# Kernel tuning notes

Hardware: AMD Instinct MI355X
Metric: run time of the kernel (lower is better)

The kernel has to match this reference:

```python
import jax, jax.numpy as jnp
import numpy as np

DIM = 192
N_HEADS = 8
HEAD_DIM = DIM // N_HEADS
SCALE = 1.0 / np.sqrt(HEAD_DIM).astype(np.float32)
H_GRID, W_GRID = 32, 64
KH, KW = 7, 11


def build_local_mask():
    # Equivalent to the torch double-loop construction: token (h2,w2) may attend
    # to (h,w) iff |h2-h| <= KH//2 and |w2-w| <= KW//2 (odd kernels).
    hh = jnp.arange(H_GRID)
    ww = jnp.arange(W_GRID)
    dh_ok = jnp.abs(hh[:, None] - hh[None, :]) <= KH // 2  # [H, H]
    dw_ok = jnp.abs(ww[:, None] - ww[None, :]) <= KW // 2  # [W, W]
    allowed = dh_ok[:, None, :, None] & dw_ok[None, :, None, :]  # [H, W, H, W]
    allowed = allowed.reshape(H_GRID * W_GRID, H_GRID * W_GRID)
    return jnp.where(allowed, 0.0, -jnp.inf).astype(jnp.float32)  # [N, N]


def setup_inputs() -> dict:
    key = jax.random.key(0)
    ks = jax.random.split(key, 5)
    B, N = 4, H_GRID * W_GRID
    w_std = 1.0 / np.sqrt(DIM)
    x = jax.random.normal(ks[0], (B, N, DIM), dtype=jnp.float32)
    qkv_w = jax.random.normal(ks[1], (3 * DIM, DIM), dtype=jnp.float32) * w_std
    qkv_b = jax.random.normal(ks[2], (3 * DIM,), dtype=jnp.float32) * 0.02
    proj_w = jax.random.normal(ks[3], (DIM, DIM), dtype=jnp.float32) * w_std
    proj_b = jax.random.normal(ks[4], (DIM,), dtype=jnp.float32) * 0.02
    mask = build_local_mask()
    return {"x": x, "qkv_w": qkv_w, "qkv_b": qkv_b,
            "proj_w": proj_w, "proj_b": proj_b, "mask": mask}


def reference(x, qkv_w, qkv_b, proj_w, proj_b, mask):
    B, N, _ = x.shape
    qkv = x @ qkv_w.T + qkv_b                              # [B, N, 3*DIM]
    qkv = qkv.reshape(B, N, 3, N_HEADS, HEAD_DIM)
    qkv = jnp.transpose(qkv, (2, 0, 3, 1, 4))              # [3, B, h, N, d]
    q, k, v = qkv[0] * SCALE, qkv[1], qkv[2]
    attn = jnp.einsum('bhnd,bhmd->bhnm', q, k) + mask      # [B, h, N, N]
    attn = jax.nn.softmax(attn, axis=-1)                   # == log_softmax().exp()
    out = jnp.einsum('bhnm,bhmd->bhnd', attn, v)           # [B, h, N, d]
    out = jnp.transpose(out, (0, 2, 1, 3)).reshape(B, N, DIM)
    return out @ proj_w.T + proj_b
```

## Files before the change

kernel.cpp:

```cpp
#include <hip/hip_runtime.h>
#include <math.h>

#define H_GRID 32
#define W_GRID 64
#define NTOK   2048
#define NHEADS 8
#define HD     24
#define DIMC   192
#define BATCH  4

static constexpr float SCALE = 0.20412414523193154f;

typedef unsigned short ushort;
typedef unsigned int   uint;
typedef __attribute__((ext_vector_type(8))) _Float16 f16x8;
typedef __attribute__((ext_vector_type(4))) float    f32x4;

static __device__ __forceinline__ float4 ld4(const float* p) { return *(const float4*)p; }

static __device__ __forceinline__ ushort f2h(float f) {
    _Float16 h = (_Float16)f;
    union { _Float16 h; ushort u; } c; c.h = h; return c.u;
}
static __device__ __forceinline__ float h2f(ushort u) {
    union { ushort u; _Float16 h; } c; c.u = u; return (float)c.h;
}

__global__ __launch_bounds__(256) void cast_h(const float* __restrict__ x,
                                              const float* __restrict__ wq,
                                              const float* __restrict__ wp,
                                              ushort* __restrict__ xh,
                                              ushort* __restrict__ wqh,
                                              ushort* __restrict__ wph,
                                              ushort* __restrict__ Qh,
                                              ushort* __restrict__ Kh) {
    const int i = blockIdx.x * 256 + threadIdx.x;
    if (i >= 430080) {
        const int ti = i - 430080;
        ushort* dst = (ti >> 16) ? Kh : Qh;
        const int row = ti & 65535;
        const uint4 z = {0u, 0u, 0u, 0u};
        *(uint4*)&dst[(size_t)row * 32 + 24] = z;
        return;
    }
    const float* src; ushort* dh; int off;
    if (i < 393216)      { src = x;  dh = xh;  off = i; }
    else if (i < 420864) { src = wq; dh = wqh; off = i - 393216; }
    else                 { src = wp; dh = wph; off = i - 420864; }
    float4 v = ld4(src + (size_t)off * 4);
    *(ushort4*)(dh + (size_t)off * 4) =
        make_ushort4(f2h(v.x), f2h(v.y), f2h(v.z), f2h(v.w));
}

__global__ __launch_bounds__(256) void gemm_qkv(const ushort* __restrict__ Ah,
                                                const ushort* __restrict__ Wh,
                                                const float* __restrict__ bias,
                                                ushort* __restrict__ Qh,
                                                ushort* __restrict__ Kh,
                                                ushort* __restrict__ VTh) {
    __shared__ ushort Ws[64 * 200];

    const int t    = threadIdx.x;
    const int wave = t >> 6, lane = t & 63;
    const int m0   = blockIdx.x * 64 + wave * 16;
    const int j0   = blockIdx.y * 64;
    const int n16  = lane & 15;
    const int kq   = lane >> 4;

    for (int i = t; i < 1536; i += 256) {
        const int r = i / 24, c = i - (i / 24) * 24;
        *(uint4*)&Ws[r * 200 + c * 8] = *(const uint4*)&Wh[(size_t)(j0 + r) * 192 + c * 8];
    }

    const ushort* ap = Ah + (size_t)(m0 + n16) * 192 + kq * 8;

    f32x4 acc[4] = {f32x4{0,0,0,0}, f32x4{0,0,0,0}, f32x4{0,0,0,0}, f32x4{0,0,0,0}};

    __syncthreads();

#pragma unroll
    for (int ks = 0; ks < 6; ks++) {
        const f16x8 af = *(const f16x8*)(ap + ks * 32);
#pragma unroll
        for (int nt = 0; nt < 4; nt++) {
            const f16x8 bf = *(const f16x8*)&Ws[(nt * 16 + n16) * 200 + kq * 8 + ks * 32];
            acc[nt] = __builtin_amdgcn_mfma_f32_16x16x32_f16(af, bf, acc[nt], 0, 0, 0);
        }
    }

    const int band = blockIdx.y / 3;
    const int mrow0 = m0 + kq * 4;
    const int b_    = mrow0 >> 11;
    const int tok0  = mrow0 & 2047;

    if (band == 2) {
#pragma unroll
        for (int nt = 0; nt < 4; nt++) {
            const int col = j0 + nt * 16 + n16;
            const int lc  = col - 384;
            const int h_  = lc / 24;
            const int d_  = lc - h_ * 24;
            const float bv = bias[col];
            ushort vv[4];
#pragma unroll
            for (int r = 0; r < 4; r++) vv[r] = f2h(acc[nt][r] + bv);
            const size_t addr = ((size_t)(b_ * 8 + h_) * 32 + d_) * 2080 + 8 + tok0;
            *(ushort4*)&VTh[addr] = make_ushort4(vv[0], vv[1], vv[2], vv[3]);
        }
    } else {
        const float sc_ = band ? 1.0f : SCALE;
        __syncthreads();
#pragma unroll
        for (int nt = 0; nt < 4; nt++) {
            const int col = j0 + nt * 16 + n16;
            const float bv = bias[col];
#pragma unroll
            for (int r = 0; r < 4; r++) {
                Ws[(wave * 16 + kq * 4 + r) * 68 + nt * 16 + n16] =
                    f2h((acc[nt][r] + bv) * sc_);
            }
        }
        __syncthreads();
        ushort* dst = band ? Kh : Qh;
        const int lc0 = j0 - band * 192;
#pragma unroll
        for (int it = 0; it < 4; it++) {
            const int item = t + 256 * it;
            const int tokl = item >> 4;
            const int cg   = item & 15;
            const ushort4 v = *(const ushort4*)&Ws[tokl * 68 + cg * 4];
            const int lc = lc0 + cg * 4;
            const int h_ = lc / 24;
            const int d0 = lc - h_ * 24;
            const int m  = blockIdx.x * 64 + tokl;
            const size_t addr = ((size_t)((m >> 11) * 8 + h_) * 2048 + (m & 2047)) * 32 + d0;
            *(ushort4*)&dst[addr] = v;
        }
    }
}

__global__ __launch_bounds__(256) void attn_mfma(const ushort* __restrict__ Qh,
                                                 const ushort* __restrict__ Kh,
                                                 const ushort* __restrict__ VTh,
                                                 ushort* __restrict__ aws) {
    const int qtile = blockIdx.x;
    const int head  = blockIdx.y;
    const int b     = blockIdx.z;
    const int qh0   = (qtile >> 3) * 4;
    const int qw0   = (qtile & 7) * 8;
    const int kw0a  = qw0 - 8;

    const int t = threadIdx.x;
    const int w = t >> 6, lane = t & 63;
    const int n16 = lane & 15, quad = lane >> 4;
    const int bh = b * 8 + head;

    __shared__ ushort P[32 * 328];
    __shared__ ushort Os[32 * 28];
    __shared__ float  mxbuf[64], sumbuf[64];

    const ushort* Qb = Qh + (size_t)bh * 65536;
    const ushort* Kb = Kh + (size_t)bh * 65536;

    const int mt = w >> 1, nth = w & 1;
    const int mrow = 16 * mt + n16;
    const int tq_a = ((qh0 + (mrow >> 3)) << 6) + qw0 + (mrow & 7);
    const f16x8 qf = *(const f16x8*)&Qb[(size_t)tq_a * 32 + quad * 8];

    float sv[10][4];
    float mx4[4] = {-3e38f, -3e38f, -3e38f, -3e38f};
#pragma unroll
    for (int j = 0; j < 10; j++) {
        const int slot = (nth * 10 + j) * 16 + n16;
        const int rr = slot >> 5, cc = slot & 31;
        const int khv = qh0 - 3 + rr;
        const int kwv = kw0a + cc;
        const int tok = (min(max(khv, 0), 31) << 6) + min(max(kwv, 0), 63);
        const f16x8 kf = *(const f16x8*)&Kb[(size_t)tok * 32 + quad * 8];
        f32x4 a = f32x4{0, 0, 0, 0};
        a = __builtin_amdgcn_mfma_f32_16x16x32_f16(qf, kf, a, 0, 0, 0);
        const bool kok = (khv >= 0) && (khv < 32) && (kwv >= 0) && (kwv < 64);
#pragma unroll
        for (int r = 0; r < 4; r++) {
            const int m   = 16 * mt + quad * 4 + r;
            const int qhv = qh0 + (m >> 3);
            const int qwv = qw0 + (m & 7);
            const bool valid = kok && (abs(khv - qhv) <= 3) && (abs(kwv - qwv) <= 5);
            const float s = valid ? a[r] : -3e38f;
            sv[j][r] = s;
            mx4[r] = fmaxf(mx4[r], s);
        }
    }
#pragma unroll
    for (int d = 1; d < 16; d <<= 1)
#pragma unroll
        for (int r = 0; r < 4; r++) mx4[r] = fmaxf(mx4[r], __shfl_xor(mx4[r], d));
    if (n16 == 0) {
#pragma unroll
        for (int r = 0; r < 4; r++) mxbuf[w * 16 + quad * 4 + r] = mx4[r];
    }
    __syncthreads();
#pragma unroll
    for (int r = 0; r < 4; r++) mx4[r] = fmaxf(mx4[r], mxbuf[(w ^ 1) * 16 + quad * 4 + r]);

    float sum4[4] = {0.f, 0.f, 0.f, 0.f};
#pragma unroll
    for (int j = 0; j < 10; j++) {
        const int slot = (nth * 10 + j) * 16 + n16;
#pragma unroll
        for (int r = 0; r < 4; r++) {
            const float p = __expf(sv[j][r] - mx4[r]);
            const ushort ph = f2h(p);
            sum4[r] += h2f(ph);
            P[(16 * mt + quad * 4 + r) * 328 + slot] = ph;
        }
    }
#pragma unroll
    for (int d = 1; d < 16; d <<= 1)
#pragma unroll
        for (int r = 0; r < 4; r++) sum4[r] += __shfl_xor(sum4[r], d);
    if (n16 == 0) {
#pragma unroll
        for (int r = 0; r < 4; r++) sumbuf[w * 16 + quad * 4 + r] = sum4[r];
    }
    __syncthreads();

    const int mtP = w >> 1, ntP = w & 1;
    const int dcol = 16 * ntP + n16;
    const ushort* VTb = VTh + (size_t)bh * 32 * 2080;
    f32x4 acc = f32x4{0, 0, 0, 0};
#pragma unroll
    for (int ks = 0; ks < 10; ks++) {
        const int kh_cl = min(max(qh0 - 3 + ks, 0), 31);
        const f16x8 pa = *(const f16x8*)&P[(16 * mtP + n16) * 328 + ks * 32 + quad * 8];
        const f16x8 vf = *(const f16x8*)&VTb[(size_t)dcol * 2080 + 8 + (kh_cl << 6) + kw0a + quad * 8];
        acc = __builtin_amdgcn_mfma_f32_16x16x32_f16(pa, vf, acc, 0, 0, 0);
    }
    if (dcol < 24) {
#pragma unroll
        for (int r = 0; r < 4; r++) {
            const int m = 16 * mtP + quad * 4 + r;
            const float tot = sumbuf[(2 * mtP) * 16 + (m & 15)] +
                              sumbuf[(2 * mtP + 1) * 16 + (m & 15)];
            Os[m * 28 + dcol] = f2h(acc[r] / tot);
        }
    }
    __syncthreads();

    if (t < 192) {
        const int tok = t / 6, g = t - (t / 6) * 6;
        const ushort4 v = *(const ushort4*)&Os[tok * 28 + g * 4];
        const int tq = ((qh0 + (tok >> 3)) << 6) + qw0 + (tok & 7);
        *(ushort4*)&aws[((size_t)(b * 2048 + tq)) * 192 + head * 24 + g * 4] = v;
    }
}

__global__ __launch_bounds__(128) void gemm_proj(const ushort* __restrict__ Ah,
                                                 const ushort* __restrict__ Wh,
                                                 const float* __restrict__ bias,
                                                 float* __restrict__ C) {
    __shared__ ushort Ws[64 * 200];

    const int t    = threadIdx.x;
    const int wave = t >> 6, lane = t & 63;
    const int m0   = blockIdx.x * 32 + wave * 16;
    const int j0   = blockIdx.y * 64;
    const int n16  = lane & 15;
    const int kq   = lane >> 4;

    for (int i = t; i < 1536; i += 128) {
        const int r = i / 24, c = i - (i / 24) * 24;
        *(uint4*)&Ws[r * 200 + c * 8] = *(const uint4*)&Wh[(size_t)(j0 + r) * 192 + c * 8];
    }

    const ushort* ap = Ah + (size_t)(m0 + n16) * 192 + kq * 8;

    f32x4 acc[4] = {f32x4{0,0,0,0}, f32x4{0,0,0,0}, f32x4{0,0,0,0}, f32x4{0,0,0,0}};

    __syncthreads();

#pragma unroll
    for (int ks = 0; ks < 6; ks++) {
        const f16x8 af = *(const f16x8*)(ap + ks * 32);
#pragma unroll
        for (int nt = 0; nt < 4; nt++) {
            const f16x8 bf = *(const f16x8*)&Ws[(nt * 16 + n16) * 200 + kq * 8 + ks * 32];
            acc[nt] = __builtin_amdgcn_mfma_f32_16x16x32_f16(af, bf, acc[nt], 0, 0, 0);
        }
    }

#pragma unroll
    for (int nt = 0; nt < 4; nt++) {
        const int col = j0 + nt * 16 + n16;
        const float bv = bias[col];
#pragma unroll
        for (int r = 0; r < 4; r++) {
            const int m = m0 + kq * 4 + r;
            C[(size_t)m * 192 + col] = acc[nt][r] + bv;
        }
    }
}

extern "C" void kernel_launch(void* const* d_in, const int* in_sizes, int n_in,
                              void* d_out, int out_size, void* d_ws, size_t ws_size,
                              hipStream_t stream) {
    const float* x      = (const float*)d_in[0];
    const float* qkv_w  = (const float*)d_in[1];
    const float* qkv_b  = (const float*)d_in[2];
    const float* proj_w = (const float*)d_in[3];
    const float* proj_b = (const float*)d_in[4];

    char* wsb = (char*)d_ws;
    ushort* xh   = (ushort*)(wsb + 0);
    ushort* wqh  = (ushort*)(wsb + 3145728);
    ushort* wph  = (ushort*)(wsb + 3366912);
    ushort* Qh   = (ushort*)(wsb + 3440640);
    ushort* Kh   = (ushort*)(wsb + 7634944);
    ushort* VTh  = (ushort*)(wsb + 11829248);
    ushort* awsh = (ushort*)(wsb + 16171008);
    float*  out  = (float*)d_out;

    hipLaunchKernelGGL(cast_h, dim3(2192), dim3(256), 0, stream,
                       x, qkv_w, proj_w, xh, wqh, wph, Qh, Kh);
    hipLaunchKernelGGL(gemm_qkv, dim3(128, 9), dim3(256), 0, stream,
                       xh, wqh, qkv_b, Qh, Kh, VTh);
    hipLaunchKernelGGL(attn_mfma, dim3(64, 8, 4), dim3(256), 0, stream,
                       Qh, Kh, VTh, awsh);
    hipLaunchKernelGGL(gemm_proj, dim3(256, 3), dim3(128), 0, stream,
                       awsh, wph, proj_b, out);
}
```

Measured before the change: 115.2 us.

## Stage K and V tiles in LDS for attention, prefetch A fragments in GEMMs

The attention kernel now cooperatively loads the 320-token K window and the V^T window into shared memory before the MMA loops, and reuses the K buffer for the probability matrix. Previously each wave gathered K and V fragments straight from global memory with clamped indices. The two GEMMs load all A fragments into registers before the barrier so those global loads overlap the weight staging, and launch_bounds occupancy hints are added. Costs are more LDS per block and higher register pressure, which may limit occupancy.

```diff
diff --git a/kernel.cpp b/kernel.cpp
--- a/kernel.cpp
+++ b/kernel.cpp
@@ -52,12 +52,12 @@
         make_ushort4(f2h(v.x), f2h(v.y), f2h(v.z), f2h(v.w));
 }
 
-__global__ __launch_bounds__(256) void gemm_qkv(const ushort* __restrict__ Ah,
-                                                const ushort* __restrict__ Wh,
-                                                const float* __restrict__ bias,
-                                                ushort* __restrict__ Qh,
-                                                ushort* __restrict__ Kh,
-                                                ushort* __restrict__ VTh) {
+__global__ __launch_bounds__(256, 4) void gemm_qkv(const ushort* __restrict__ Ah,
+                                                   const ushort* __restrict__ Wh,
+                                                   const float* __restrict__ bias,
+                                                   ushort* __restrict__ Qh,
+                                                   ushort* __restrict__ Kh,
+                                                   ushort* __restrict__ VTh) {
     __shared__ ushort Ws[64 * 200];
 
     const int t    = threadIdx.x;
@@ -74,21 +74,24 @@
 
     const ushort* ap = Ah + (size_t)(m0 + n16) * 192 + kq * 8;
 
+    f16x8 af[6];
+#pragma unroll
+    for (int ks = 0; ks < 6; ks++) af[ks] = *(const f16x8*)(ap + ks * 32);
+
     f32x4 acc[4] = {f32x4{0,0,0,0}, f32x4{0,0,0,0}, f32x4{0,0,0,0}, f32x4{0,0,0,0}};
 
     __syncthreads();
 
 #pragma unroll
     for (int ks = 0; ks < 6; ks++) {
-        const f16x8 af = *(const f16x8*)(ap + ks * 32);
 #pragma unroll
         for (int nt = 0; nt < 4; nt++) {
             const f16x8 bf = *(const f16x8*)&Ws[(nt * 16 + n16) * 200 + kq * 8 + ks * 32];
-            acc[nt] = __builtin_amdgcn_mfma_f32_16x16x32_f16(af, bf, acc[nt], 0, 0, 0);
-        }
-    }
-
-    const int band = blockIdx.y / 3;
+            acc[nt] = __builtin_amdgcn_mfma_f32_16x16x32_f16(af[ks], bf, acc[nt], 0, 0, 0);
+        }
+    }
+
+    const int band  = blockIdx.y / 3;
     const int mrow0 = m0 + kq * 4;
     const int b_    = mrow0 >> 11;
     const int tok0  = mrow0 & 2047;
@@ -139,10 +142,10 @@
     }
 }
 
-__global__ __launch_bounds__(256) void attn_mfma(const ushort* __restrict__ Qh,
-                                                 const ushort* __restrict__ Kh,
-                                                 const ushort* __restrict__ VTh,
-                                                 ushort* __restrict__ aws) {
+__global__ __launch_bounds__(256, 3) void attn_mfma(const ushort* __restrict__ Qh,
+                                                    const ushort* __restrict__ Kh,
+                                                    const ushort* __restrict__ VTh,
+                                                    ushort* __restrict__ aws) {
     const int qtile = blockIdx.x;
     const int head  = blockIdx.y;
     const int b     = blockIdx.z;
@@ -155,17 +158,37 @@
     const int n16 = lane & 15, quad = lane >> 4;
     const int bh = b * 8 + head;
 
-    __shared__ ushort P[32 * 328];
+    __shared__ ushort KP[320 * 36];
+    __shared__ ushort VTs[32 * 328];
     __shared__ ushort Os[32 * 28];
     __shared__ float  mxbuf[64], sumbuf[64];
 
-    const ushort* Qb = Qh + (size_t)bh * 65536;
-    const ushort* Kb = Kh + (size_t)bh * 65536;
+    const ushort* Qb  = Qh  + (size_t)bh * 65536;
+    const ushort* Kb  = Kh  + (size_t)bh * 65536;
+    const ushort* VTb = VTh + (size_t)bh * 66560;
+
+    for (int i = t; i < 1280; i += 256) {
+        const int slot = i >> 2, part = i & 3;
+        const int rr = slot >> 5, cc = slot & 31;
+        const int khv = qh0 - 3 + rr;
+        const int kwv = kw0a + cc;
+        const int tok = (min(max(khv, 0), 31) << 6) + min(max(kwv, 0), 63);
+        *(uint4*)&KP[slot * 36 + part * 8] = *(const uint4*)&Kb[(size_t)tok * 32 + part * 8];
+    }
+    for (int i = t; i < 1280; i += 256) {
+        const int d = i / 40, rem = i - d * 40;
+        const int rr = rem >> 2, chunk = rem & 3;
+        const int kh_cl = min(max(qh0 - 3 + rr, 0), 31);
+        const ushort* src = VTb + (size_t)d * 2080 + 8 + (kh_cl << 6) + kw0a + chunk * 8;
+        *(uint4*)&VTs[d * 328 + rr * 32 + chunk * 8] = *(const uint4*)src;
+    }
 
     const int mt = w >> 1, nth = w & 1;
     const int mrow = 16 * mt + n16;
     const int tq_a = ((qh0 + (mrow >> 3)) << 6) + qw0 + (mrow & 7);
     const f16x8 qf = *(const f16x8*)&Qb[(size_t)tq_a * 32 + quad * 8];
+
+    __syncthreads();
 
     float sv[10][4];
     float mx4[4] = {-3e38f, -3e38f, -3e38f, -3e38f};
@@ -175,8 +198,7 @@
         const int rr = slot >> 5, cc = slot & 31;
         const int khv = qh0 - 3 + rr;
         const int kwv = kw0a + cc;
-        const int tok = (min(max(khv, 0), 31) << 6) + min(max(kwv, 0), 63);
-        const f16x8 kf = *(const f16x8*)&Kb[(size_t)tok * 32 + quad * 8];
+        const f16x8 kf = *(const f16x8*)&KP[slot * 36 + quad * 8];
         f32x4 a = f32x4{0, 0, 0, 0};
         a = __builtin_amdgcn_mfma_f32_16x16x32_f16(qf, kf, a, 0, 0, 0);
         const bool kok = (khv >= 0) && (khv < 32) && (kwv >= 0) && (kwv < 64);
@@ -212,7 +234,7 @@
             const float p = __expf(sv[j][r] - mx4[r]);
             const ushort ph = f2h(p);
             sum4[r] += h2f(ph);
-            P[(16 * mt + quad * 4 + r) * 328 + slot] = ph;
+            KP[(16 * mt + quad * 4 + r) * 328 + slot] = ph;
         }
     }
 #pragma unroll
@@ -227,13 +249,11 @@
 
     const int mtP = w >> 1, ntP = w & 1;
     const int dcol = 16 * ntP + n16;
-    const ushort* VTb = VTh + (size_t)bh * 32 * 2080;
     f32x4 acc = f32x4{0, 0, 0, 0};
 #pragma unroll
     for (int ks = 0; ks < 10; ks++) {
-        const int kh_cl = min(max(qh0 - 3 + ks, 0), 31);
-        const f16x8 pa = *(const f16x8*)&P[(16 * mtP + n16) * 328 + ks * 32 + quad * 8];
-        const f16x8 vf = *(const f16x8*)&VTb[(size_t)dcol * 2080 + 8 + (kh_cl << 6) + kw0a + quad * 8];
+        const f16x8 pa = *(const f16x8*)&KP[(16 * mtP + n16) * 328 + ks * 32 + quad * 8];
+        const f16x8 vf = *(const f16x8*)&VTs[dcol * 328 + ks * 32 + quad * 8];
         acc = __builtin_amdgcn_mfma_f32_16x16x32_f16(pa, vf, acc, 0, 0, 0);
     }
     if (dcol < 24) {
@@ -255,10 +275,10 @@
     }
 }
 
-__global__ __launch_bounds__(128) void gemm_proj(const ushort* __restrict__ Ah,
-                                                 const ushort* __restrict__ Wh,
-                                                 const float* __restrict__ bias,
-                                                 float* __restrict__ C) {
+__global__ __launch_bounds__(128, 4) void gemm_proj(const ushort* __restrict__ Ah,
+                                                    const ushort* __restrict__ Wh,
+                                                    const float* __restrict__ bias,
+                                                    float* __restrict__ C) {
     __shared__ ushort Ws[64 * 200];
 
     const int t    = threadIdx.x;
@@ -275,17 +295,20 @@
 
     const ushort* ap = Ah + (size_t)(m0 + n16) * 192 + kq * 8;
 
+    f16x8 af[6];
+#pragma unroll
+    for (int ks = 0; ks < 6; ks++) af[ks] = *(const f16x8*)(ap + ks * 32);
+
     f32x4 acc[4] = {f32x4{0,0,0,0}, f32x4{0,0,0,0}, f32x4{0,0,0,0}, f32x4{0,0,0,0}};
 
     __syncthreads();
 
 #pragma unroll
     for (int ks = 0; ks < 6; ks++) {
-        const f16x8 af = *(const f16x8*)(ap + ks * 32);
 #pragma unroll
         for (int nt = 0; nt < 4; nt++) {
             const f16x8 bf = *(const f16x8*)&Ws[(nt * 16 + n16) * 200 + kq * 8 + ks * 32];
-            acc[nt] = __builtin_amdgcn_mfma_f32_16x16x32_f16(af, bf, acc[nt], 0, 0, 0);
+            acc[nt] = __builtin_amdgcn_mfma_f32_16x16x32_f16(af[ks], bf, acc[nt], 0, 0, 0);
         }
     }
 
```

Result: slower. 121.8 us (+5.7%).
